# Optimization experiments

Measured on AMD Instinct MI355X. Metric: run time of the kernel, lower is better.

Reference implementation:

```python
import jax, jax.numpy as jnp
import numpy as np

B, C, H, W, KS = 8, 3, 512, 512, 3
K = KS * KS  # kernel_elements = 9


def setup_inputs() -> dict:
    key = jax.random.key(0)
    ks = jax.random.split(key, 5)
    return {
        "x": jax.random.normal(ks[0], (B, C, H, W), jnp.float32),
        "w1": jax.random.normal(ks[1], (K - 1, C, KS, KS), jnp.float32) * 0.1,  # find_ref conv weight
        "b1": jax.random.normal(ks[2], (K - 1,), jnp.float32) * 0.1,
        "w2": jax.random.normal(ks[3], (C, K), jnp.float32) * 0.1,  # grouped 1x1 conv: C groups, K in-ch each
        "b2": jax.random.normal(ks[4], (C,), jnp.float32) * 0.1,
    }


def _grid_sample_bilinear(img_nhwc, gx, gy):
    # torch.grid_sample, mode='bilinear', padding_mode='zeros', align_corners=False
    # img_nhwc: [B,H,W,C]; gx,gy: [B,h,w,K] normalized coords (x=width, y=height)
    Bs, Hh, Ww, _ = img_nhwc.shape
    ix = ((gx + 1.0) * Ww - 1.0) * 0.5
    iy = ((gy + 1.0) * Hh - 1.0) * 0.5
    ix0 = jnp.floor(ix)
    iy0 = jnp.floor(iy)
    wx1 = ix - ix0
    wy1 = iy - iy0
    wx0 = 1.0 - wx1
    wy0 = 1.0 - wy1
    bidx = jnp.arange(Bs)[:, None, None, None]

    def corner(yc, xc, wgt):
        valid = (xc >= 0) & (xc < Ww) & (yc >= 0) & (yc < Hh)
        xi = jnp.clip(xc, 0, Ww - 1).astype(jnp.int32)
        yi = jnp.clip(yc, 0, Hh - 1).astype(jnp.int32)
        v = img_nhwc[bidx, yi, xi]  # [B,h,w,K,C]
        return v * (wgt * valid)[..., None]

    out = corner(iy0, ix0, wy0 * wx0)
    out = out + corner(iy0, ix0 + 1.0, wy0 * wx1)
    out = out + corner(iy0 + 1.0, ix0, wy1 * wx0)
    out = out + corner(iy0 + 1.0, ix0 + 1.0, wy1 * wx1)
    return out  # [B,h,w,K,C]


def _forward(x, w1, b1, w2, b2):
    Bs, Cc, Hh, Ww = x.shape
    pad = KS // 2
    # find_ref: conv3x3 (pad=1) + sigmoid -> offsets in [0,1]
    off = jax.lax.conv_general_dilated(
        x, w1, (1, 1), ((pad, pad), (pad, pad)),
        dimension_numbers=("NCHW", "OIHW", "NCHW"))
    off = jax.nn.sigmoid(off + b1[None, :, None, None])  # [B,K-1,H,W]
    off = jnp.transpose(off, (0, 2, 3, 1)).reshape(Bs, Hh, Ww, (K - 1) // 2, 2)
    ctr = float(KS // 2)
    sym = 2.0 * ctr - off  # find_symmetric_points
    center = jnp.zeros((Bs, Hh, Ww, 1, 2), off.dtype)
    off_all = jnp.concatenate([off, center, sym], axis=-2)  # [B,H,W,K,2]
    # base grid: stack(h_grid, w_grid) with linspace(0,1)
    base = jnp.stack(
        jnp.meshgrid(jnp.linspace(0.0, 1.0, Hh), jnp.linspace(0.0, 1.0, Ww), indexing="ij"),
        axis=-1)  # [H,W,2]
    coords = base[None, :, :, None, :] + off_all  # [B,H,W,K,2]
    # grid_sample interprets last dim as (x=width, y=height)
    gx = coords[..., 0]
    gy = coords[..., 1]
    img = jnp.transpose(x, (0, 2, 3, 1))  # [B,H,W,C]
    sampled = _grid_sample_bilinear(img, gx, gy)  # [B,H,W,K,C]
    # concatenation order in torch: elem-major channels -> [B, K*C, H, W]
    deformed = jnp.transpose(sampled, (0, 3, 4, 1, 2)).reshape(Bs, K * Cc, Hh, Ww)
    # grouped 1x1 conv: groups=C, group g consumes channels [g*K:(g+1)*K]
    grp = deformed.reshape(Bs, Cc, K, Hh, Ww)
    out = jnp.einsum("bgkhw,gk->bghw", grp, w2) + b2[None, :, None, None]
    return jax.nn.relu(out)


def reference(x, w1, b1, w2, b2):
    return _forward(x, w1, b1, w2, b2)
```

## Files before the change

kernel.cpp:

```cpp
#include <hip/hip_runtime.h>

#define BATCH 8
#define HDIM  512
#define WDIM  512
#define PLANE (HDIM * WDIM)

typedef _Float16 half2v __attribute__((ext_vector_type(2)));
typedef _Float16 half8v __attribute__((ext_vector_type(8)));
typedef float    f2v    __attribute__((ext_vector_type(2)));

struct __align__(8) HQuad { half2v p0, p1, p2, p3; };

#if __has_builtin(__builtin_amdgcn_fdot2)
#define FDOT2(a, b, c) __builtin_amdgcn_fdot2((a), (b), (c), false)
#else
#define FDOT2(a, b, c) fmaf((float)(a).x, (float)(b).x, fmaf((float)(a).y, (float)(b).y, (c)))
#endif

#if __has_builtin(__builtin_amdgcn_exp2f)
#define EXP2F(x) __builtin_amdgcn_exp2f(x)
#else
#define EXP2F(x) exp2f(x)
#endif

__global__ __launch_bounds__(256) void repack_h4x(
    const float* __restrict__ x,
    half8v* __restrict__ xp)
{
    int b = blockIdx.x & 7;
    int u = ((blockIdx.x >> 3) << 8) + threadIdx.x;
    const float* xb = x + (size_t)b * 3 * PLANE;
    int pix = u << 2;
    float4 a0 = *(const float4*)(xb + pix);
    float4 a1 = *(const float4*)(xb + PLANE + pix);
    float4 a2 = *(const float4*)(xb + 2 * PLANE + pix);
    half8v o0, o1;
    o0[0] = (_Float16)a0.x; o0[1] = (_Float16)a1.x; o0[2] = (_Float16)a2.x; o0[3] = (_Float16)0.f;
    o0[4] = (_Float16)a0.y; o0[5] = (_Float16)a1.y; o0[6] = (_Float16)a2.y; o0[7] = (_Float16)0.f;
    o1[0] = (_Float16)a0.z; o1[1] = (_Float16)a1.z; o1[2] = (_Float16)a2.z; o1[3] = (_Float16)0.f;
    o1[4] = (_Float16)a0.w; o1[5] = (_Float16)a1.w; o1[6] = (_Float16)a2.w; o1[7] = (_Float16)0.f;
    size_t base = (size_t)b * (PLANE / 2) + (size_t)u * 2;
    xp[base]     = o0;
    xp[base + 1] = o1;
}

__global__ __launch_bounds__(256) void seesaw_v8(
    const float* __restrict__ x,
    const char* __restrict__ xpack,
    const float* __restrict__ w1, const float* __restrict__ b1,
    const float* __restrict__ w2, const float* __restrict__ b2,
    float* __restrict__ out)
{
    int t = threadIdx.x;
    int b    = blockIdx.x & 7;
    int rest = blockIdx.x >> 3;
    int i    = rest >> 1;
    int j    = ((rest & 1) << 8) + t;

    const float* xb = x + (size_t)b * 3 * PLANE;
    const char*  hb = xpack + ((size_t)b << 21);

    float v[27];
    int cm1 = j - 1; if (cm1 < 0) cm1 = 0;
    int cp1 = j + 1; if (cp1 > 511) cp1 = 511;
    bool jlo = (j == 0), jhi = (j == 511);

    if (i >= 1 && i <= 510) {
#pragma unroll
        for (int di = 0; di < 3; di++) {
            const float* row = xb + ((i + di - 1) << 9);
#pragma unroll
            for (int c = 0; c < 3; c++) {
                const float* rc = row + c * PLANE;
                float vm = rc[cm1]; if (jlo) vm = 0.f;
                float v0 = rc[j];
                float vp = rc[cp1]; if (jhi) vp = 0.f;
                v[c * 9 + di * 3 + 0] = vm;
                v[c * 9 + di * 3 + 1] = v0;
                v[c * 9 + di * 3 + 2] = vp;
            }
        }
    } else {
#pragma unroll
        for (int di = 0; di < 3; di++) {
            int y = i + di - 1;
            bool yv = (unsigned)y < (unsigned)HDIM;
            const float* row = xb + ((yv ? y : 0) << 9);
#pragma unroll
            for (int c = 0; c < 3; c++) {
                const float* rc = row + c * PLANE;
                float vm = rc[cm1]; if (jlo || !yv) vm = 0.f;
                float v0 = rc[j];   if (!yv)        v0 = 0.f;
                float vp = rc[cp1]; if (jhi || !yv) vp = 0.f;
                v[c * 9 + di * 3 + 0] = vm;
                v[c * 9 + di * 3 + 1] = v0;
                v[c * 9 + di * 3 + 2] = vp;
            }
        }
    }

    f2v V[13];
#pragma unroll
    for (int k = 0; k < 13; k++) { V[k][0] = v[2 * k]; V[k][1] = v[2 * k + 1]; }

    float acc[8];
#pragma unroll
    for (int e = 0; e < 8; e++) {
        const float* we = w1 + e * 27;
        f2v a2; a2[0] = b1[e]; a2[1] = 0.f;
#pragma unroll
        for (int k = 0; k < 13; k++) {
            f2v ww; ww[0] = we[2 * k]; ww[1] = we[2 * k + 1];
            a2 = __builtin_elementwise_fma(V[k], ww, a2);
        }
        acc[e] = a2[0] + a2[1] + v[26] * we[26];
    }

    const float NLOG2E = -1.44269504f;
    float s256[8];
#pragma unroll
    for (int e = 0; e < 8; e++)
        s256[e] = 256.0f * __builtin_amdgcn_rcpf(1.0f + EXP2F(acc[e] * NLOG2E));

    half2v w2a[5], w2b[5];
#pragma unroll
    for (int q = 0; q < 5; q++) {
        w2a[q][0] = (_Float16)w2[q * 3];
        w2a[q][1] = (_Float16)w2[q * 3 + 1];
        w2b[q][0] = (_Float16)w2[q * 3 + 2];
        w2b[q][1] = (_Float16)0.f;
    }

    const float k511 = 256.0f / 511.0f;
    float fxb = fmaf((float)i, k511, 255.5f);
    float fyb = fmaf((float)j, k511, 255.5f);

    int   adr[5][2];
    float wY0[5], wY1[5], wX0[5], wX1[5];
#pragma unroll
    for (int q = 0; q < 5; q++) {
        float ixf = (q < 4) ? (fxb + s256[2 * q])     : fxb;
        float iyf = (q < 4) ? (fyb + s256[2 * q + 1]) : fyb;
        float wx1 = ixf - truncf(ixf);
        float wy1 = iyf - truncf(iyf);
        int ix0 = (int)ixf, iy0 = (int)iyf;
        float wx0 = 1.f - wx1, wy0 = 1.f - wy1;

        float wx0v = (ix0 <= 511) ? wx0 : 0.f;
        float wx1v = (ix0 <= 510) ? wx1 : 0.f;
        float wy0v = (iy0 <= 511) ? wy0 : 0.f;
        float wy1v = (iy0 <= 510) ? wy1 : 0.f;
        int x0c = min(ix0, 511);
        int y0c = min(iy0, 511), y1c = min(iy0 + 1, 511);

        float wxs = wx0v + wx1v;
        wX0[q] = wx0v; wX1[q] = wx1v;
        wY0[q] = wy0v; wY1[q] = wy1v;
        adr[q][0] = (wy0v * wxs > 0.f) ? ((y0c << 9) + x0c) : 0;
        adr[q][1] = (wy1v * wxs > 0.f) ? ((y1c << 9) + x0c) : 0;
    }

    HQuad qv[5][2];
#pragma unroll
    for (int q = 0; q < 5; q++) {
        qv[q][0] = *(const HQuad*)(hb + ((size_t)adr[q][0] << 3));
        qv[q][1] = *(const HQuad*)(hb + ((size_t)adr[q][1] << 3));
    }

    float og[3] = {0.f, 0.f, 0.f};
#pragma unroll
    for (int q = 0; q < 5; q++) {
        int g = q / 3;
        float dl0 = FDOT2(qv[q][0].p0, w2a[q], FDOT2(qv[q][0].p1, w2b[q], 0.f));
        float dh0 = FDOT2(qv[q][0].p2, w2a[q], FDOT2(qv[q][0].p3, w2b[q], 0.f));
        float dl1 = FDOT2(qv[q][1].p0, w2a[q], FDOT2(qv[q][1].p1, w2b[q], 0.f));
        float dh1 = FDOT2(qv[q][1].p2, w2a[q], FDOT2(qv[q][1].p3, w2b[q], 0.f));
        float r0 = fmaf(dh0, wX1[q], dl0 * wX0[q]);
        float r1 = fmaf(dh1, wX1[q], dl1 * wX0[q]);
        og[g] = fmaf(r1, wY1[q], fmaf(r0, wY0[q], og[g]));
    }

    if ((i | j) == 0) {
#pragma unroll
        for (int p = 5; p < 9; p++) {
            float ixf = fxb + 512.0f - s256[2 * (p - 5)];
            float iyf = fyb + 512.0f - s256[2 * (p - 5) + 1];
            float ix0f = floorf(ixf), iy0f = floorf(iyf);
            float wx1 = ixf - ix0f, wy1 = iyf - iy0f;
            float wx0 = 1.f - wx1,  wy0 = 1.f - wy1;
            int ix0 = (int)ix0f, iy0 = (int)iy0f;
            float s0 = 0.f, s1 = 0.f, s2 = 0.f;
            for (int cy = 0; cy < 2; cy++) {
                int yc2 = iy0 + cy;
                if (yc2 < 0 || yc2 >= HDIM) continue;
                float wy = cy ? wy1 : wy0;
                for (int cx = 0; cx < 2; cx++) {
                    int xcc2 = ix0 + cx;
                    if (xcc2 < 0 || xcc2 >= WDIM) continue;
                    float wgt = wy * (cx ? wx1 : wx0);
                    int base = (yc2 << 9) + xcc2;
                    s0 = fmaf(xb[base],             wgt, s0);
                    s1 = fmaf(xb[PLANE + base],     wgt, s1);
                    s2 = fmaf(xb[2 * PLANE + base], wgt, s2);
                }
            }
            int g  = p / 3;
            int k0 = (p % 3) * 3;
            og[g] = fmaf(s0, w2[g * 9 + k0 + 0], og[g]);
            og[g] = fmaf(s1, w2[g * 9 + k0 + 1], og[g]);
            og[g] = fmaf(s2, w2[g * 9 + k0 + 2], og[g]);
        }
    }

    size_t ob = (size_t)(b * 3) * PLANE + ((size_t)i << 9) + j;
#pragma unroll
    for (int g = 0; g < 3; g++) {
        float vv = og[g] + b2[g];
        out[ob + (size_t)g * PLANE] = vv > 0.f ? vv : 0.f;
    }
}

__global__ __launch_bounds__(256) void seesaw_fused_v1(
    const float* __restrict__ x, const float* __restrict__ w1,
    const float* __restrict__ b1, const float* __restrict__ w2,
    const float* __restrict__ b2, float* __restrict__ out)
{
    int t = threadIdx.x;
    int gid = blockIdx.x * 256 + t;
    int j = gid & (WDIM - 1);
    int i = (gid >> 9) & (HDIM - 1);
    int b = gid >> 18;
    const float* xb = x + (size_t)b * 3 * PLANE;
    float acc[8];
#pragma unroll
    for (int e = 0; e < 8; e++) acc[e] = b1[e];
#pragma unroll
    for (int di = 0; di < 3; di++) {
        int y = i + di - 1;
        if (y < 0 || y >= HDIM) continue;
#pragma unroll
        for (int dj = 0; dj < 3; dj++) {
            int xc = j + dj - 1;
            if (xc < 0 || xc >= WDIM) continue;
            size_t base = (size_t)y * WDIM + xc;
#pragma unroll
            for (int c = 0; c < 3; c++) {
                float v = xb[(size_t)c * PLANE + base];
#pragma unroll
                for (int e = 0; e < 8; e++)
                    acc[e] = fmaf(v, w1[e * 27 + c * 9 + di * 3 + dj], acc[e]);
            }
        }
    }
    float s[8];
#pragma unroll
    for (int e = 0; e < 8; e++) s[e] = 1.0f / (1.0f + __expf(-acc[e]));
    const float inv511 = 1.0f / 511.0f;
    float bx = (float)i * inv511, by = (float)j * inv511;
    float og0 = 0.f, og1 = 0.f, og2 = 0.f;
#pragma unroll
    for (int p = 0; p < 9; p++) {
        float c0, c1;
        if (p < 4)       { c0 = s[2 * p];              c1 = s[2 * p + 1]; }
        else if (p == 4) { c0 = 0.f;                   c1 = 0.f; }
        else             { c0 = 2.0f - s[2 * (p - 5)]; c1 = 2.0f - s[2 * (p - 5) + 1]; }
        float ixf = (bx + c0) * 256.0f + 255.5f;
        float iyf = (by + c1) * 256.0f + 255.5f;
        float ix0f = floorf(ixf), iy0f = floorf(iyf);
        float wx1 = ixf - ix0f, wy1 = iyf - iy0f;
        float wx0 = 1.f - wx1,  wy0 = 1.f - wy1;
        int ix0 = (int)ix0f, iy0 = (int)iy0f;
        float s0 = 0.f, s1 = 0.f, s2 = 0.f;
#pragma unroll
        for (int cy = 0; cy < 2; cy++) {
            int yc = iy0 + cy;
            if (yc < 0 || yc >= HDIM) continue;
            float wy = cy ? wy1 : wy0;
#pragma unroll
            for (int cx = 0; cx < 2; cx++) {
                int xcc = ix0 + cx;
                if (xcc < 0 || xcc >= WDIM) continue;
                float wgt = wy * (cx ? wx1 : wx0);
                size_t base = (size_t)yc * WDIM + xcc;
                s0 = fmaf(xb[base],             wgt, s0);
                s1 = fmaf(xb[PLANE + base],     wgt, s1);
                s2 = fmaf(xb[2 * PLANE + base], wgt, s2);
            }
        }
        int g  = p / 3;
        int k0 = (p % 3) * 3;
        float* og = (g == 0) ? &og0 : (g == 1) ? &og1 : &og2;
        *og = fmaf(s0, w2[g * 9 + k0 + 0], *og);
        *og = fmaf(s1, w2[g * 9 + k0 + 1], *og);
        *og = fmaf(s2, w2[g * 9 + k0 + 2], *og);
    }
    size_t ob = (size_t)(b * 3) * PLANE + (size_t)i * WDIM + j;
    float v0 = og0 + b2[0], v1 = og1 + b2[1], v2 = og2 + b2[2];
    out[ob]             = v0 > 0.f ? v0 : 0.f;
    out[ob + PLANE]     = v1 > 0.f ? v1 : 0.f;
    out[ob + 2 * PLANE] = v2 > 0.f ? v2 : 0.f;
}

extern "C" void kernel_launch(void* const* d_in, const int* in_sizes, int n_in,
                              void* d_out, int out_size, void* d_ws, size_t ws_size,
                              hipStream_t stream) {
    const float* x  = (const float*)d_in[0];
    const float* w1 = (const float*)d_in[1];
    const float* b1 = (const float*)d_in[2];
    const float* w2 = (const float*)d_in[3];
    const float* b2 = (const float*)d_in[4];
    float* out = (float*)d_out;

    int total = BATCH * HDIM * WDIM;
    size_t need = (size_t)total * 8 + 16;

    if (ws_size >= need) {
        repack_h4x<<<total / 4 / 256, 256, 0, stream>>>(x, (half8v*)d_ws);
        seesaw_v8<<<total / 256, 256, 0, stream>>>(x, (const char*)d_ws,
                                                   w1, b1, w2, b2, out);
    } else {
        seesaw_fused_v1<<<total / 256, 256, 0, stream>>>(x, w1, b1, w2, b2, out);
    }
}
```

Measured before the change: 128.4 us.

## Repack only the reachable bottom-right quadrant into a transposed half4 texture

The repack kernel now converts only the 256x256 quadrant of the image that the sigmoid-bounded sample coordinates can reach. It stores that quadrant transposed in a column-major fp16 layout, so the paired bilinear corners are adjacent along y instead of x. The gather kernel's addressing and weight order are changed to match, out-of-range samples point at a dead texel, and the center tap at edge pixels is handled by a separate fp32 path. The aim is to cut repack traffic and workspace size and to improve gather locality, at the cost of relying on the coordinate range analysis and adding edge-case branches.

```diff
diff --git a/kernel.cpp b/kernel.cpp
--- a/kernel.cpp
+++ b/kernel.cpp
@@ -5,8 +5,11 @@
 #define WDIM  512
 #define PLANE (HDIM * WDIM)
 
+#define QDIM      256
+#define DEAD_TEX  65535
+
 typedef _Float16 half2v __attribute__((ext_vector_type(2)));
-typedef _Float16 half8v __attribute__((ext_vector_type(8)));
+typedef _Float16 half4v __attribute__((ext_vector_type(4)));
 typedef float    f2v    __attribute__((ext_vector_type(2)));
 
 struct __align__(8) HQuad { half2v p0, p1, p2, p3; };
@@ -23,28 +26,34 @@
 #define EXP2F(x) exp2f(x)
 #endif
 
-__global__ __launch_bounds__(256) void repack_h4x(
+__global__ __launch_bounds__(256) void repack_tq(
     const float* __restrict__ x,
-    half8v* __restrict__ xp)
+    half4v* __restrict__ hp)
 {
     int b = blockIdx.x & 7;
     int u = ((blockIdx.x >> 3) << 8) + threadIdx.x;
+    int xq = u & 63;
+    int yr = u >> 6;
+    int xcol = QDIM + (xq << 2);
+    int off  = ((QDIM + yr) << 9) + xcol;
     const float* xb = x + (size_t)b * 3 * PLANE;
-    int pix = u << 2;
-    float4 a0 = *(const float4*)(xb + pix);
-    float4 a1 = *(const float4*)(xb + PLANE + pix);
-    float4 a2 = *(const float4*)(xb + 2 * PLANE + pix);
-    half8v o0, o1;
-    o0[0] = (_Float16)a0.x; o0[1] = (_Float16)a1.x; o0[2] = (_Float16)a2.x; o0[3] = (_Float16)0.f;
-    o0[4] = (_Float16)a0.y; o0[5] = (_Float16)a1.y; o0[6] = (_Float16)a2.y; o0[7] = (_Float16)0.f;
-    o1[0] = (_Float16)a0.z; o1[1] = (_Float16)a1.z; o1[2] = (_Float16)a2.z; o1[3] = (_Float16)0.f;
-    o1[4] = (_Float16)a0.w; o1[5] = (_Float16)a1.w; o1[6] = (_Float16)a2.w; o1[7] = (_Float16)0.f;
-    size_t base = (size_t)b * (PLANE / 2) + (size_t)u * 2;
-    xp[base]     = o0;
-    xp[base + 1] = o1;
+    float4 a0 = *(const float4*)(xb + off);
+    float4 a1 = *(const float4*)(xb + PLANE + off);
+    float4 a2 = *(const float4*)(xb + 2 * PLANE + off);
+    size_t base = ((size_t)b << 16) + yr;
+    float c0[4] = {a0.x, a0.y, a0.z, a0.w};
+    float c1[4] = {a1.x, a1.y, a1.z, a1.w};
+    float c2[4] = {a2.x, a2.y, a2.z, a2.w};
+#pragma unroll
+    for (int k = 0; k < 4; k++) {
+        half4v o;
+        o[0] = (_Float16)c0[k]; o[1] = (_Float16)c1[k];
+        o[2] = (_Float16)c2[k]; o[3] = (_Float16)0.f;
+        hp[base + (((size_t)(xq * 4 + k)) << 8)] = o;
+    }
 }
 
-__global__ __launch_bounds__(256) void seesaw_v8(
+__global__ __launch_bounds__(256) void seesaw_v10(
     const float* __restrict__ x,
     const char* __restrict__ xpack,
     const float* __restrict__ w1, const float* __restrict__ b1,
@@ -58,7 +67,7 @@
     int j    = ((rest & 1) << 8) + t;
 
     const float* xb = x + (size_t)b * 3 * PLANE;
-    const char*  hb = xpack + ((size_t)b << 21);
+    const char*  hb = xpack + ((size_t)b << 19);
 
     float v[27];
     int cm1 = j - 1; if (cm1 < 0) cm1 = 0;
@@ -134,9 +143,10 @@
     const float k511 = 256.0f / 511.0f;
     float fxb = fmaf((float)i, k511, 255.5f);
     float fyb = fmaf((float)j, k511, 255.5f);
+    bool c_edge = (i == 0) || (j == 0);
 
     int   adr[5][2];
-    float wY0[5], wY1[5], wX0[5], wX1[5];
+    float wXa[5], wXb[5], wYa[5], wYb[5];
 #pragma unroll
     for (int q = 0; q < 5; q++) {
         float ixf = (q < 4) ? (fxb + s256[2 * q])     : fxb;
@@ -150,14 +160,18 @@
         float wx1v = (ix0 <= 510) ? wx1 : 0.f;
         float wy0v = (iy0 <= 511) ? wy0 : 0.f;
         float wy1v = (iy0 <= 510) ? wy1 : 0.f;
-        int x0c = min(ix0, 511);
-        int y0c = min(iy0, 511), y1c = min(iy0 + 1, 511);
-
-        float wxs = wx0v + wx1v;
-        wX0[q] = wx0v; wX1[q] = wx1v;
-        wY0[q] = wy0v; wY1[q] = wy1v;
-        adr[q][0] = (wy0v * wxs > 0.f) ? ((y0c << 9) + x0c) : 0;
-        adr[q][1] = (wy1v * wxs > 0.f) ? ((y1c << 9) + x0c) : 0;
+        if (q == 4 && c_edge) { wx0v = 0.f; wx1v = 0.f; }
+
+        int x0c = min(ix0, 511);     x0c = max(x0c, QDIM);
+        int x1c = min(ix0 + 1, 511); x1c = max(x1c, QDIM);
+        int y0c = min(iy0, 511);     y0c = max(y0c, QDIM);
+        int yce = y0c - QDIM;
+
+        float wys = wy0v + wy1v;
+        wXa[q] = wx0v; wXb[q] = wx1v;
+        wYa[q] = wy0v; wYb[q] = wy1v;
+        adr[q][0] = (wx0v * wys > 0.f) ? (((x0c - QDIM) << 8) + yce) : DEAD_TEX;
+        adr[q][1] = (wx1v * wys > 0.f) ? (((x1c - QDIM) << 8) + yce) : DEAD_TEX;
     }
 
     HQuad qv[5][2];
@@ -171,13 +185,41 @@
 #pragma unroll
     for (int q = 0; q < 5; q++) {
         int g = q / 3;
-        float dl0 = FDOT2(qv[q][0].p0, w2a[q], FDOT2(qv[q][0].p1, w2b[q], 0.f));
-        float dh0 = FDOT2(qv[q][0].p2, w2a[q], FDOT2(qv[q][0].p3, w2b[q], 0.f));
-        float dl1 = FDOT2(qv[q][1].p0, w2a[q], FDOT2(qv[q][1].p1, w2b[q], 0.f));
-        float dh1 = FDOT2(qv[q][1].p2, w2a[q], FDOT2(qv[q][1].p3, w2b[q], 0.f));
-        float r0 = fmaf(dh0, wX1[q], dl0 * wX0[q]);
-        float r1 = fmaf(dh1, wX1[q], dl1 * wX0[q]);
-        og[g] = fmaf(r1, wY1[q], fmaf(r0, wY0[q], og[g]));
+        float a0 = FDOT2(qv[q][0].p0, w2a[q], FDOT2(qv[q][0].p1, w2b[q], 0.f));
+        float a1 = FDOT2(qv[q][0].p2, w2a[q], FDOT2(qv[q][0].p3, w2b[q], 0.f));
+        float b0 = FDOT2(qv[q][1].p0, w2a[q], FDOT2(qv[q][1].p1, w2b[q], 0.f));
+        float b1d = FDOT2(qv[q][1].p2, w2a[q], FDOT2(qv[q][1].p3, w2b[q], 0.f));
+        float rA = fmaf(a1, wYb[q], a0 * wYa[q]);
+        float rB = fmaf(b1d, wYb[q], b0 * wYa[q]);
+        og[g] = fmaf(rB, wXb[q], fmaf(rA, wXa[q], og[g]));
+    }
+
+    if (c_edge) {
+        float ixf = fxb, iyf = fyb;
+        float ix0f = floorf(ixf), iy0f = floorf(iyf);
+        float wx1 = ixf - ix0f, wy1 = iyf - iy0f;
+        float wx0 = 1.f - wx1,  wy0 = 1.f - wy1;
+        int ix0 = (int)ix0f, iy0 = (int)iy0f;
+        float s0 = 0.f, s1 = 0.f, s2 = 0.f;
+#pragma unroll
+        for (int cy = 0; cy < 2; cy++) {
+            int yc2 = iy0 + cy;
+            if (yc2 < 0 || yc2 >= HDIM) continue;
+            float wy = cy ? wy1 : wy0;
+#pragma unroll
+            for (int cx = 0; cx < 2; cx++) {
+                int xcc2 = ix0 + cx;
+                if (xcc2 < 0 || xcc2 >= WDIM) continue;
+                float wgt = wy * (cx ? wx1 : wx0);
+                int base = (yc2 << 9) + xcc2;
+                s0 = fmaf(xb[base],             wgt, s0);
+                s1 = fmaf(xb[PLANE + base],     wgt, s1);
+                s2 = fmaf(xb[2 * PLANE + base], wgt, s2);
+            }
+        }
+        og[1] = fmaf(s0, w2[12], og[1]);
+        og[1] = fmaf(s1, w2[13], og[1]);
+        og[1] = fmaf(s2, w2[14], og[1]);
     }
 
     if ((i | j) == 0) {
@@ -312,12 +354,12 @@
     float* out = (float*)d_out;
 
     int total = BATCH * HDIM * WDIM;
-    size_t need = (size_t)total * 8 + 16;
+    size_t need = ((size_t)BATCH << 19) + 32;
 
     if (ws_size >= need) {
-        repack_h4x<<<total / 4 / 256, 256, 0, stream>>>(x, (half8v*)d_ws);
-        seesaw_v8<<<total / 256, 256, 0, stream>>>(x, (const char*)d_ws,
-                                                   w1, b1, w2, b2, out);
+        repack_tq<<<512, 256, 0, stream>>>(x, (half4v*)d_ws);
+        seesaw_v10<<<total / 256, 256, 0, stream>>>(x, (const char*)d_ws,
+                                                    w1, b1, w2, b2, out);
     } else {
         seesaw_fused_v1<<<total / 256, 256, 0, stream>>>(x, w1, b1, w2, b2, out);
     }
```

After: 124.9 us. 2.7% less time.
